# Performance work log

Hardware: AMD Instinct MI355X
Metric: run time of the kernel (lower is better)

The kernel has to match this reference:

```python
import jax, jax.numpy as jnp
import numpy as np
import math

B, T, C = 2, 1024, 1024
H = 16
HS = C // H          # head size 64
ROT = HS // 2        # rotary dims 32
TT = 1024            # ctx_len
FFN = 4 * C
EPS = 1e-6


def _layernorm(x, g, b):
    m = jnp.mean(x, -1, keepdims=True)
    v = jnp.mean((x - m) ** 2, -1, keepdims=True)
    return (x - m) * jax.lax.rsqrt(v + EPS) * g + b


def _time_shift_half(x):
    # ZeroPad2d((0,0,1,-1)) applied to first half of channels: shift by one step in time
    c = x.shape[-1]
    a = jnp.pad(x[:, :, : c // 2], ((0, 0), (1, 0), (0, 0)))[:, :-1, :]
    return jnp.concatenate([a, x[:, :, c // 2 :]], axis=-1)


def _rotate_half(x):
    x1, x2 = jnp.split(x, 2, axis=-1)
    return jnp.concatenate([-x2, x1], axis=-1)


def _rotary_cos_sin(t_len, rot, base):
    inv_freq = 1.0 / (base ** (jnp.arange(0, rot, 2, dtype=jnp.float32) / rot))
    freqs = jnp.arange(t_len, dtype=jnp.float32)[:, None] * inv_freq[None, :]
    emb = jnp.concatenate([freqs, freqs], axis=-1)  # (T, rot)
    return jnp.cos(emb), jnp.sin(emb)


def _build_w(time_w, time_alpha, time_beta, t_len):
    # faithful translation of the pad/tile/reshape circulant trick
    w = jnp.pad(time_w, ((0, 0), (0, TT)))            # (H, 2TT)
    w = jnp.tile(w, (1, TT))                          # (H, 2TT*TT)
    w = w[:, :-TT].reshape(-1, TT, 2 * TT - 1)        # (H, TT, 2TT-1)
    w = w[:, :, TT - 1 :]                             # (H, TT, TT)
    return w[:, :t_len, :t_len] * time_alpha[:, :, :t_len] * time_beta[:, :t_len, :]


def setup_inputs() -> dict:
    key = jax.random.key(0)
    ks = jax.random.split(key, 24)
    s = 0.02
    d = {
        "x": jax.random.normal(ks[0], (B, T, C), jnp.float32),
        "ln1_g": jnp.ones((C,), jnp.float32),
        "ln1_b": jnp.zeros((C,), jnp.float32),
        "Wq": jax.random.normal(ks[1], (C, C), jnp.float32) * s,
        "bq": jnp.zeros((C,), jnp.float32),
        "Wk": jax.random.normal(ks[2], (C, C), jnp.float32) * s,
        "bk": jnp.zeros((C,), jnp.float32),
        "Wv": jax.random.normal(ks[3], (C, C), jnp.float32) * s,
        "bv": jnp.zeros((C,), jnp.float32),
        "Wo": jax.random.normal(ks[4], (C, C), jnp.float32) * s,
        "bo": jnp.zeros((C,), jnp.float32),
        "time_w": 1.0 + 0.01 * jax.random.normal(ks[5], (H, TT), jnp.float32),
        "time_alpha": 1.0 + 0.01 * jax.random.normal(ks[6], (H, 1, TT), jnp.float32),
        "time_beta": 1.0 + 0.01 * jax.random.normal(ks[7], (H, TT, 1), jnp.float32),
        "time_gamma": 1.0 + 0.01 * jax.random.normal(ks[8], (TT, 1), jnp.float32),
        "Wmix": jnp.eye(H, dtype=jnp.float32) + 0.01 * jax.random.normal(ks[9], (H, H), jnp.float32),
        "ln2_g": jnp.ones((C,), jnp.float32),
        "ln2_b": jnp.zeros((C,), jnp.float32),
        "Wgk": jax.random.normal(ks[10], (C, FFN), jnp.float32) * s,
        "bgk": jnp.zeros((FFN,), jnp.float32),
        "Wgv": jax.random.normal(ks[11], (C, FFN), jnp.float32) * s,
        "bgv": jnp.zeros((FFN,), jnp.float32),
        "Wgw": jax.random.normal(ks[12], (FFN, C), jnp.float32) * s,
        "bgw": jnp.zeros((C,), jnp.float32),
    }
    return d


def _block(x, ln1_g, ln1_b, Wq, bq, Wk, bk, Wv, bv, Wo, bo,
           time_w, time_alpha, time_beta, time_gamma, Wmix,
           ln2_g, ln2_b, Wgk, bgk, Wgv, bgv, Wgw, bgw):
    b, t, c = x.shape
    # ---- MHA_pro attention sublayer (pre-LN residual) ----
    xs = _time_shift_half(_layernorm(x, ln1_g, ln1_b))
    q = (xs @ Wq + bq).reshape(b, t, H, HS).transpose(0, 2, 1, 3)  # bhtd
    k = (xs @ Wk + bk).reshape(b, t, H, HS).transpose(0, 2, 1, 3)
    v = (xs @ Wv + bv).reshape(b, t, H, HS).transpose(0, 2, 1, 3)
    qr, qp = q[..., :ROT], q[..., ROT:]
    kr, kp = k[..., :ROT], k[..., ROT:]
    cos, sin = _rotary_cos_sin(t, ROT, float(TT))  # base = ctx_len
    qr = qr * cos + _rotate_half(qr) * sin
    kr = kr * cos + _rotate_half(kr) * sin
    q = jnp.concatenate([qr, qp], axis=-1)
    k = jnp.concatenate([kr, kp], axis=-1)
    att = jnp.einsum("bhtd,bhud->bhtu", q, k) * (1.0 / math.sqrt(HS))
    causal = jnp.tril(jnp.ones((t, t), bool))
    att = jnp.where(causal, att, -jnp.inf)
    att = jax.nn.softmax(att, axis=-1)
    w = _build_w(time_w, time_alpha, time_beta, t)  # (H, T, T)
    att = att * w[None]
    att = jnp.einsum("ij,bjtu->bitu", Wmix, att)  # 1x1 conv head mix
    y = jnp.einsum("bhtu,bhud->bhtd", att, v)
    y = y.transpose(0, 2, 1, 3).reshape(b, t, c)
    y = (y @ Wo + bo) * time_gamma[:t, :]
    x = x + y
    # ---- GeGLU MLP sublayer (pre-LN residual) ----
    xm = _layernorm(x, ln2_g, ln2_b)
    kk = xm @ Wgk + bgk
    vv = xm @ Wgv + bgv
    y2 = (jax.nn.gelu(kk, approximate=False) * vv) @ Wgw + bgw
    return x + y2


def reference(x, ln1_g, ln1_b, Wq, bq, Wk, bk, Wv, bv, Wo, bo,
              time_w, time_alpha, time_beta, time_gamma, Wmix,
              ln2_g, ln2_b, Wgk, bgk, Wgv, bgv, Wgw, bgw):
    return _block(x, ln1_g, ln1_b, Wq, bq, Wk, bk, Wv, bv, Wo, bo,
                  time_w, time_alpha, time_beta, time_gamma, Wmix,
                  ln2_g, ln2_b, Wgk, bgk, Wgv, bgv, Wgw, bgw)
```

## Files before the change

kernel.cpp:

```cpp
#include <hip/hip_runtime.h>
#include <math.h>

typedef unsigned short u16;
typedef short s16x8 __attribute__((ext_vector_type(8)));
typedef float f32x4 __attribute__((ext_vector_type(4)));

#define TB 2
#define TSEQ 1024
#define CC 1024
#define NH 16
#define HSZ 64
#define FFN 4096
#define MROWS (TB*TSEQ)

#define GLOAD16(g, l) __builtin_amdgcn_global_load_lds( \
    (const __attribute__((address_space(1))) unsigned*)(g), \
    (__attribute__((address_space(3))) unsigned*)(l), 16, 0, 0)

#define SBAR()  __builtin_amdgcn_s_barrier()
#define SCHED0() __builtin_amdgcn_sched_barrier(0)
#define LGKM0() asm volatile("s_waitcnt lgkmcnt(0)" ::: "memory")
#define WAITV4() asm volatile("s_waitcnt vmcnt(4)" ::: "memory")
#define PRIO(n) __builtin_amdgcn_s_setprio(n)

__device__ __forceinline__ float bf2f(u16 u){
  union { unsigned u; float f; } c; c.u = ((unsigned)u) << 16; return c.f;
}
__device__ __forceinline__ u16 f2bf(float f){
  union { float f; unsigned u; } c; c.f = f;
  unsigned u = c.u;
  u += 0x7fffu + ((u >> 16) & 1);
  return (u16)(u >> 16);
}
__device__ __forceinline__ float ldin(const void* p, size_t i, int bf){
  return bf ? bf2f(((const u16*)p)[i]) : ((const float*)p)[i];
}

__global__ void k_flag(const unsigned* __restrict__ g, int* __restrict__ flag){
  if (threadIdx.x == 0) *flag = (g[0] == 0x3F800000u) ? 0 : 1;
}

struct Prep {
  const void* csrc[10]; u16* cdst[10]; int cp0[11];
  const void* tw; u16* tw8; float2* rt;
};
__global__ void k_prep(Prep P, const int* __restrict__ flagp){
  int bf = *flagp;
  int blk = blockIdx.x, tid = threadIdx.x;
  if (blk < 184){
    int idx = blk*256 + tid;
    int s = 0;
    #pragma unroll
    for (int i = 1; i < 10; i++) if (idx >= P.cp0[i]) s = i;
    int r = idx - P.cp0[s];
    P.cdst[s][r] = f2bf(ldin(P.csrc[s], r, bf));
  } else if (blk < 696){
    int idx = (blk-184)*256 + tid;
    int s = idx >> 14;
    int h = (idx >> 10) & 15;
    int k = idx & 1023;
    float v = (k + s < 1024) ? ldin(P.tw, h*1024 + k + s, bf) : 0.f;
    P.tw8[idx] = f2bf(v);
  } else {
    int idx = (blk-696)*256 + tid;
    int i = idx & 15, t = idx >> 4;
    float invf = exp2f(-0.625f * (float)i);
    float ang = (float)t * invf;
    P.rt[idx] = (float2){cosf(ang), sinf(ang)};
  }
}

struct TEnt { const void* src; u16* dst; int R, C, bxn, blk0; };
struct TPack { TEnt e[7]; };
__global__ void k_transpose_all(TPack p, const int* __restrict__ flagp){
  int bf = *flagp;
  __shared__ u16 tile[32][33];
  int blk = blockIdx.x;
  int ei = 0;
  #pragma unroll
  for (int i = 1; i < 7; i++) if (blk >= p.e[i].blk0) ei = i;
  const void* src = p.e[ei].src;
  u16* dst = p.e[ei].dst;
  int R = p.e[ei].R, C = p.e[ei].C;
  int rel = blk - p.e[ei].blk0;
  int bx = (rel % p.e[ei].bxn) * 32, by = (rel / p.e[ei].bxn) * 32;
  int tx = threadIdx.x & 31, ty = threadIdx.x >> 5;
  #pragma unroll
  for (int i = 0; i < 32; i += 8)
    tile[ty + i][tx] = f2bf(ldin(src, (size_t)(by + ty + i) * C + bx + tx, bf));
  __syncthreads();
  #pragma unroll
  for (int i = 0; i < 32; i += 8)
    dst[(size_t)(bx + ty + i) * R + by + tx] = tile[tx][ty + i];
}

__global__ void k_ln1_shift(const void* __restrict__ x, const void* __restrict__ g,
                            const void* __restrict__ bta, u16* __restrict__ xs,
                            const int* __restrict__ flagp){
  int bf = *flagp;
  int row = blockIdx.x;
  int t = row & (TSEQ - 1);
  int tid = threadIdx.x;
  int wv = tid >> 6, lane = tid & 63;
  float v[4]; float s = 0.f, ss = 0.f;
  #pragma unroll
  for (int i = 0; i < 4; i++){
    v[i] = ldin(x, (size_t)row * CC + tid*4 + i, bf);
    s += v[i]; ss += v[i]*v[i];
  }
  #pragma unroll
  for (int o = 32; o > 0; o >>= 1){ s += __shfl_xor(s, o); ss += __shfl_xor(ss, o); }
  __shared__ float rs[4], rss[4];
  if (lane == 0){ rs[wv] = s; rss[wv] = ss; }
  __syncthreads();
  float S = rs[0]+rs[1]+rs[2]+rs[3];
  float SS = rss[0]+rss[1]+rss[2]+rss[3];
  float mean = S * (1.0f/CC);
  float var  = SS * (1.0f/CC) - mean*mean;
  float inv  = rsqrtf(var + 1e-6f);
  #pragma unroll
  for (int i = 0; i < 4; i++){
    int c = tid*4 + i;
    float o = (v[i]-mean)*inv*ldin(g, c, bf) + ldin(bta, c, bf);
    u16 ob = f2bf(o);
    if (c >= CC/2)            xs[(size_t)row*CC + c] = ob;
    else if (t < TSEQ-1)      xs[(size_t)(row+1)*CC + c] = ob;
  }
  if (t == 0 && tid < 128){
    #pragma unroll
    for (int i = 0; i < 4; i++) xs[(size_t)row*CC + tid*4 + i] = 0;
  }
}

__global__ void k_ln2(const float* __restrict__ x1, const void* __restrict__ g,
                      const void* __restrict__ bta, u16* __restrict__ xm,
                      const int* __restrict__ flagp){
  int bf = *flagp;
  int row = blockIdx.x;
  int tid = threadIdx.x;
  int wv = tid >> 6, lane = tid & 63;
  const float* xr = x1 + (size_t)row * CC;
  float v[4]; float s = 0.f, ss = 0.f;
  #pragma unroll
  for (int i = 0; i < 4; i++){ v[i] = xr[tid*4 + i]; s += v[i]; ss += v[i]*v[i]; }
  #pragma unroll
  for (int o = 32; o > 0; o >>= 1){ s += __shfl_xor(s, o); ss += __shfl_xor(ss, o); }
  __shared__ float rs[4], rss[4];
  if (lane == 0){ rs[wv] = s; rss[wv] = ss; }
  __syncthreads();
  float S = rs[0]+rs[1]+rs[2]+rs[3];
  float SS = rss[0]+rss[1]+rss[2]+rss[3];
  float mean = S * (1.0f/CC);
  float var  = SS * (1.0f/CC) - mean*mean;
  float inv  = rsqrtf(var + 1e-6f);
  #pragma unroll
  for (int i = 0; i < 4; i++){
    int c = tid*4 + i;
    xm[(size_t)row*CC + c] = f2bf((v[i]-mean)*inv*ldin(g, c, bf) + ldin(bta, c, bf));
  }
}

__global__ void k_rotary(u16* __restrict__ qkv, const float2* __restrict__ rt){
  int idx = blockIdx.x*256 + threadIdx.x;
  int i = idx & 15;
  int h = (idx >> 4) & (NH-1);
  int row = idx >> 8;
  int t = row & (TSEQ-1);
  float2 cssn = rt[t*16 + i];
  float cs = cssn.x, sn = cssn.y;
  size_t base = (size_t)row * (3*CC);
  u16* qp = qkv + base + h*HSZ;
  float a = bf2f(qp[i]), b2 = bf2f(qp[i+16]);
  qp[i]    = f2bf(a*cs - b2*sn);
  qp[i+16] = f2bf(b2*cs + a*sn);
  u16* kp = qkv + base + CC + h*HSZ;
  a = bf2f(kp[i]); b2 = bf2f(kp[i+16]);
  kp[i]    = f2bf(a*cs - b2*sn);
  kp[i+16] = f2bf(b2*cs + a*sn);
}

__global__ __launch_bounds__(256) void k_qk(
    const u16* __restrict__ qkv, u16* __restrict__ att)
{
  int m0 = blockIdx.y * 128;
  int n0 = blockIdx.x * 128;
  if (n0 > m0) return;
  int bh = blockIdx.z; int b = bh >> 4, h = bh & 15;
  __shared__ u16 As[128*32];
  __shared__ u16 Bs[128*32];
  int tid = threadIdx.x;
  int w = tid >> 6;
  int lane = tid & 63;
  int wm = (w >> 1) * 64, wn = (w & 1) * 64;
  f32x4 acc[4][4];
  #pragma unroll
  for (int i = 0; i < 4; i++)
    #pragma unroll
    for (int j = 0; j < 4; j++) acc[i][j] = (f32x4){0.f,0.f,0.f,0.f};

  int rr = lane >> 2;
  int cc = lane & 3;
  const u16* gA0 = qkv + (size_t)(b*TSEQ + m0 + w*32 + rr)*(3*CC) + h*HSZ + cc*8;
  const u16* gA1 = gA0 + (size_t)16*(3*CC);
  const u16* gB0 = qkv + (size_t)(b*TSEQ + n0 + w*32 + rr)*(3*CC) + CC + h*HSZ + cc*8;
  const u16* gB1 = gB0 + (size_t)16*(3*CC);
  u16* lA0 = As + (w*32)*32;
  u16* lA1 = As + (w*32+16)*32;
  u16* lB0 = Bs + (w*32)*32;
  u16* lB1 = Bs + (w*32+16)*32;
  int quad = lane >> 4;
  int l15 = lane & 15;

  #pragma unroll
  for (int k0 = 0; k0 < HSZ; k0 += 32){
    __syncthreads();
    GLOAD16(gA0 + k0, lA0);
    GLOAD16(gA1 + k0, lA1);
    GLOAD16(gB0 + k0, lB0);
    GLOAD16(gB1 + k0, lB1);
    __syncthreads();
    s16x8 af[4], bfr[4];
    #pragma unroll
    for (int i = 0; i < 4; i++){
      af[i]  = *(s16x8*)&As[(wm + i*16 + l15)*32 + quad*8];
      bfr[i] = *(s16x8*)&Bs[(wn + i*16 + l15)*32 + quad*8];
    }
    #pragma unroll
    for (int mi = 0; mi < 4; mi++)
      #pragma unroll
      for (int ni = 0; ni < 4; ni++)
        acc[mi][ni] = __builtin_amdgcn_mfma_f32_16x16x32_bf16(af[mi], bfr[ni], acc[mi][ni], 0, 0, 0);
  }

  #pragma unroll
  for (int mi = 0; mi < 4; mi++){
    int rowb = m0 + wm + mi*16 + quad*4;
    #pragma unroll
    for (int ni = 0; ni < 4; ni++){
      int col = n0 + wn + ni*16 + l15;
      #pragma unroll
      for (int r = 0; r < 4; r++){
        int t = rowb + r;
        att[((size_t)bh*TSEQ + t)*TSEQ + col] = f2bf(acc[mi][ni][r] * 0.125f);
      }
    }
  }
}

__global__ __launch_bounds__(256) void k_softmix(
    u16* __restrict__ att, const u16* __restrict__ tw8, const u16* __restrict__ al16,
    const u16* __restrict__ be16, const void* __restrict__ wmix,
    const int* __restrict__ flagp)
{
  int bf = *flagp;
  int bt = blockIdx.x;
  int t = bt & (TSEQ-1);
  int b = bt >> 10;
  int tid = threadIdx.x;
  int wv = tid >> 6;
  int lane = tid & 63;
  int tile_end = ((t >> 7) + 1) << 7;
  int nchunk = (t >> 9) + 1;
  int sh = (TSEQ-1 - t) & 7;
  int base = (TSEQ-1 - t) - sh;
  __shared__ __align__(16) u16 P[NH][TSEQ];
  __shared__ float wm[NH*NH];
  if (tid < NH*NH) wm[tid] = ldin(wmix, tid, bf);

  #pragma unroll
  for (int hi = 0; hi < 4; hi++){
    int h = wv*4 + hi;
    const u16* srow = att + ((size_t)(b*NH + h)*TSEQ + t)*TSEQ;
    const u16* twp  = tw8 + ((size_t)sh*NH + h)*TSEQ + base;
    const u16* alp  = al16 + h*TSEQ;
    float v[16];
    float lmax = -1e30f;
    for (int r = 0; r < nchunk; r++){
      int ub = lane*8 + r*512;
      uint4 pk = *(const uint4*)(srow + ub);
      const u16* pe = (const u16*)&pk;
      #pragma unroll
      for (int e = 0; e < 8; e++){
        float s = bf2f(pe[e]);
        if (ub + e > t) s = -1e30f;
        v[r*8+e] = s;
        lmax = fmaxf(lmax, s);
      }
    }
    #pragma unroll
    for (int o = 32; o > 0; o >>= 1) lmax = fmaxf(lmax, __shfl_xor(lmax, o));
    float lsum = 0.f;
    for (int r = 0; r < nchunk; r++){
      #pragma unroll
      for (int e = 0; e < 8; e++){
        float p = __expf(v[r*8+e] - lmax);
        v[r*8+e] = p; lsum += p;
      }
    }
    #pragma unroll
    for (int o = 32; o > 0; o >>= 1) lsum += __shfl_xor(lsum, o);
    float btv = bf2f(be16[h*TSEQ + t]);
    float inv = btv / lsum;
    for (int r = 0; r < nchunk; r++){
      int ub = lane*8 + r*512;
      uint4 wk = *(const uint4*)(twp + ub);
      uint4 ak = *(const uint4*)(alp + ub);
      const u16* we = (const u16*)&wk;
      const u16* ae = (const u16*)&ak;
      u16 tmp[8];
      #pragma unroll
      for (int e = 0; e < 8; e++){
        float p = v[r*8+e] * inv * bf2f(we[e]) * bf2f(ae[e]);
        tmp[e] = f2bf(p);
      }
      *(uint4*)&P[h][ub] = *(uint4*)tmp;
    }
  }
  __syncthreads();

  int u0 = tid * 4;
  if (u0 < tile_end){
    #pragma unroll
    for (int half2 = 0; half2 < 2; half2++){
      float acc[8][4];
      #pragma unroll
      for (int i = 0; i < 8; i++)
        #pragma unroll
        for (int k = 0; k < 4; k++) acc[i][k] = 0.f;
      #pragma unroll
      for (int j = 0; j < 16; j++){
        uint2 pk = *(const uint2*)&P[j][u0];
        float p0 = bf2f((u16)(pk.x & 0xffff)), p1 = bf2f((u16)(pk.x >> 16));
        float p2 = bf2f((u16)(pk.y & 0xffff)), p3 = bf2f((u16)(pk.y >> 16));
        #pragma unroll
        for (int i2 = 0; i2 < 8; i2++){
          float w = wm[(half2*8 + i2)*NH + j];
          acc[i2][0] += w*p0; acc[i2][1] += w*p1; acc[i2][2] += w*p2; acc[i2][3] += w*p3;
        }
      }
      #pragma unroll
      for (int i2 = 0; i2 < 8; i2++){
        int i = half2*8 + i2;
        u16 tmp[4] = {f2bf(acc[i2][0]), f2bf(acc[i2][1]), f2bf(acc[i2][2]), f2bf(acc[i2][3])};
        *(uint2*)(att + ((size_t)(b*NH + i)*TSEQ + t)*TSEQ + u0) = *(uint2*)tmp;
      }
    }
  }
}

__global__ void k_vt(const u16* __restrict__ qkv, u16* __restrict__ vt){
  __shared__ u16 tile[32][33];
  int bh = blockIdx.z; int b = bh >> 4, h = bh & 15;
  int u0 = blockIdx.x * 32, d0 = blockIdx.y * 32;
  int tx = threadIdx.x & 31, ty = threadIdx.x >> 5;
  #pragma unroll
  for (int i = 0; i < 32; i += 8)
    tile[ty + i][tx] = qkv[(size_t)(b*TSEQ + u0 + ty + i)*(3*CC) + 2*CC + h*HSZ + d0 + tx];
  __syncthreads();
  #pragma unroll
  for (int i = 0; i < 32; i += 8)
    vt[((size_t)bh*HSZ + d0 + ty + i)*TSEQ + u0 + tx] = tile[tx][ty + i];
}

__global__ void k_gelumul(const u16* __restrict__ kkvv, u16* __restrict__ hh){
  int idx = blockIdx.x*256 + threadIdx.x;
  int m = idx >> 9;
  int j = (idx & 511) * 8;
  uint4 kk4 = *(const uint4*)(kkvv + (size_t)m*(2*FFN) + j);
  uint4 vv4 = *(const uint4*)(kkvv + (size_t)m*(2*FFN) + FFN + j);
  const u16* ks = (const u16*)&kk4;
  const u16* vs = (const u16*)&vv4;
  u16 out[8];
  #pragma unroll
  for (int e = 0; e < 8; e++){
    float kk = bf2f(ks[e]), vv = bf2f(vs[e]);
    float ge = 0.5f*kk*(1.0f + erff(kk*0.70710678f));
    out[e] = f2bf(ge*vv);
  }
  *(uint4*)(hh + (size_t)m*FFN + j) = *(uint4*)out;
}

__global__ __launch_bounds__(512, 2) void k_gemm256(
    const u16* __restrict__ A, const u16* __restrict__ Bt,
    const u16* __restrict__ bias, int M, int N, int K, int mode,
    u16* __restrict__ outp, float* __restrict__ partial)
{
  __shared__ u16 S[65536];
  u16* SA0 = S;
  u16* SB0 = S + 16384;
  u16* SA1 = S + 32768;
  u16* SB1 = S + 49152;

  int nwg = (int)(gridDim.x * gridDim.y * gridDim.z);
  int lin = (int)(blockIdx.x + gridDim.x * (blockIdx.y + gridDim.y * blockIdx.z));
  int nl  = (nwg & 7) ? lin : ((lin & 7) * (nwg >> 3) + (lin >> 3));
  int bx  = nl % (int)gridDim.x;
  int tq  = nl / (int)gridDim.x;
  int by  = tq % (int)gridDim.y;
  int bz  = tq / (int)gridDim.y;

  int m0 = by * 256, n0 = bx * 256;
  int kper = K / (int)gridDim.z;
  int kbeg = bz * kper;
  int nt = kper >> 6;
  int niter = nt >> 1;

  int tid = threadIdx.x;
  int w = tid >> 6, lane = tid & 63;
  int wm = w >> 2, wn = w & 3;
  int quad = lane >> 4, l15 = lane & 15;
  int l3 = lane >> 3, ch = (lane & 7) ^ l3;

  const u16* gA = A  + (size_t)(m0 + w*16 + l3) * K + ch*8 + kbeg;
  const u16* gB = Bt + (size_t)(n0 + w*16 + l3) * K + ch*8 + kbeg;
  const size_t hstep = (size_t)128 * K;
  const size_t rstep = (size_t)8 * K;

  int pc0 = quad ^ (l15 & 7);
  int pc1 = (4 + quad) ^ (l15 & 7);
  int aoff0 = (wm*128 + l15)*64 + pc0*8;
  int aoff1 = (wm*128 + l15)*64 + pc1*8;
  int boff0 = (wn*64 + l15)*64 + pc0*8;
  int boff1 = (wn*64 + l15)*64 + pc1*8;

  f32x4 acc[8][4];
  #pragma unroll
  for (int i = 0; i < 8; i++)
    #pragma unroll
    for (int j = 0; j < 4; j++) acc[i][j] = (f32x4){0.f,0.f,0.f,0.f};

  #define STG(gbase, sbase, h, ko) do{ \
      const u16* _g = (gbase) + (size_t)(h)*hstep + (ko); \
      u16* _l = (sbase) + ((h)*128 + w*16)*64; \
      GLOAD16(_g, _l); \
      GLOAD16(_g + rstep, _l + 512); \
    }while(0)

  #define LD_A(buf, MQ) do{ _Pragma("unroll") for (int _m = 0; _m < 4; _m++){ \
      a0[_m] = *(const s16x8*)((buf) + aoff0 + (MQ)*4096 + _m*1024); \
      a1[_m] = *(const s16x8*)((buf) + aoff1 + (MQ)*4096 + _m*1024); } }while(0)

  #define LD_B(buf, NQ, B0A, B1A) do{ _Pragma("unroll") for (int _n = 0; _n < 2; _n++){ \
      B0A[_n] = *(const s16x8*)((buf) + boff0 + (NQ)*2048 + _n*1024); \
      B1A[_n] = *(const s16x8*)((buf) + boff1 + (NQ)*2048 + _n*1024); } }while(0)

  #define MMQ(MQ, NQ, B0A, B1A) do{ _Pragma("unroll") for (int _m = 0; _m < 4; _m++){ \
      _Pragma("unroll") for (int _n = 0; _n < 2; _n++){ \
        acc[(MQ)*4+_m][(NQ)*2+_n] = __builtin_amdgcn_mfma_f32_16x16x32_bf16(a0[_m], B0A[_n], acc[(MQ)*4+_m][(NQ)*2+_n], 0, 0, 0); \
        acc[(MQ)*4+_m][(NQ)*2+_n] = __builtin_amdgcn_mfma_f32_16x16x32_bf16(a1[_m], B1A[_n], acc[(MQ)*4+_m][(NQ)*2+_n], 0, 0, 0); }} }while(0)

  STG(gB, SB0, 0, 0); STG(gB, SB0, 1, 0);
  STG(gA, SA0, 0, 0); STG(gA, SA0, 1, 0);
  STG(gB, SB1, 0, 64); STG(gB, SB1, 1, 64);
  WAITV4();
  SBAR();

  s16x8 a0[4], a1[4], bl0[2], bl1[2], bh0[2], bh1[2];

  for (int i = 0; i < niter; i++){
    int t1k = (2*i+1)*64;
    int t2k = (2*i+2 < nt) ? (2*i+2)*64 : 0;
    int t3k = (2*i+3 < nt) ? (2*i+3)*64 : 0;

    LD_A(SA0, 0); LD_B(SB0, 0, bl0, bl1);
    STG(gA, SA1, 0, t1k);
    SBAR(); LGKM0(); SCHED0(); PRIO(1); MMQ(0,0,bl0,bl1); PRIO(0); SBAR();
    LD_B(SB0, 1, bh0, bh1);
    STG(gA, SA1, 1, t1k);
    SBAR(); LGKM0(); SCHED0(); PRIO(1); MMQ(0,1,bh0,bh1); PRIO(0); SBAR();
    LD_A(SA0, 1);
    STG(gB, SB0, 0, t2k);
    SBAR(); LGKM0(); SCHED0(); PRIO(1); MMQ(1,0,bl0,bl1); PRIO(0); SBAR();
    STG(gB, SB0, 1, t2k);
    SBAR(); LGKM0(); SCHED0(); PRIO(1); MMQ(1,1,bh0,bh1); PRIO(0);
    WAITV4(); SBAR();
    LD_A(SA1, 0); LD_B(SB1, 0, bl0, bl1);
    STG(gA, SA0, 0, t2k);
    SBAR(); LGKM0(); SCHED0(); PRIO(1); MMQ(0,0,bl0,bl1); PRIO(0); SBAR();
    LD_B(SB1, 1, bh0, bh1);
    STG(gA, SA0, 1, t2k);
    SBAR(); LGKM0(); SCHED0(); PRIO(1); MMQ(0,1,bh0,bh1); PRIO(0); SBAR();
    LD_A(SA1, 1);
    STG(gB, SB1, 0, t3k);
    SBAR(); LGKM0(); SCHED0(); PRIO(1); MMQ(1,0,bl0,bl1); PRIO(0); SBAR();
    STG(gB, SB1, 1, t3k);
    SBAR(); LGKM0(); SCHED0(); PRIO(1); MMQ(1,1,bh0,bh1); PRIO(0);
    WAITV4(); SBAR();
  }

  if (mode == 3){
    float* pout = partial + (size_t)bz * M * N;
    #pragma unroll
    for (int mi = 0; mi < 8; mi++){
      int rowb = m0 + wm*128 + mi*16 + quad*4;
      #pragma unroll
      for (int ni = 0; ni < 4; ni++){
        int col = n0 + wn*64 + ni*16 + l15;
        #pragma unroll
        for (int r = 0; r < 4; r++)
          pout[(size_t)(rowb + r) * N + col] = acc[mi][ni][r];
      }
    }
  } else {
    #pragma unroll
    for (int mi = 0; mi < 8; mi++){
      int rowb = m0 + wm*128 + mi*16 + quad*4;
      #pragma unroll
      for (int ni = 0; ni < 4; ni++){
        int col = n0 + wn*64 + ni*16 + l15;
        float bv = bf2f(bias[col]);
        #pragma unroll
        for (int r = 0; r < 4; r++)
          outp[(size_t)(rowb + r) * N + col] = f2bf(acc[mi][ni][r] + bv);
      }
    }
  }
  #undef STG
  #undef LD_A
  #undef LD_B
  #undef MMQ
}

__global__ __launch_bounds__(256) void k_gemm(
    const u16* __restrict__ A, const u16* __restrict__ Bt,
    const u16* __restrict__ bias, int M, int N, int K, int mode,
    void* __restrict__ outp, const void* __restrict__ xres,
    const float* __restrict__ resf, const u16* __restrict__ gamma,
    float* __restrict__ partial, const int* __restrict__ flagp)
{
  int bf = *flagp;
  __shared__ u16 As[128*32];
  __shared__ u16 Bs[128*32];
  int tid = threadIdx.x;
  int m0 = blockIdx.y * 128;
  int n0 = blockIdx.x * 128;
  int nz = gridDim.z;
  int kper = K / nz;
  int kbeg = blockIdx.z * kper;
  int kend = kbeg + kper;
  int w = tid >> 6;
  int lane = tid & 63;
  int wm = (w >> 1) * 64, wn = (w & 1) * 64;
  f32x4 acc[4][4];
  #pragma unroll
  for (int i = 0; i < 4; i++)
    #pragma unroll
    for (int j = 0; j < 4; j++) acc[i][j] = (f32x4){0.f,0.f,0.f,0.f};

  int rr = lane >> 2;
  int cc = lane & 3;
  const u16* gA0 = A  + (size_t)(m0 + w*32 + rr)*K + cc*8;
  const u16* gA1 = gA0 + (size_t)16*K;
  const u16* gB0 = Bt + (size_t)(n0 + w*32 + rr)*K + cc*8;
  const u16* gB1 = gB0 + (size_t)16*K;
  u16* lA0 = As + (w*32)*32;
  u16* lA1 = As + (w*32+16)*32;
  u16* lB0 = Bs + (w*32)*32;
  u16* lB1 = Bs + (w*32+16)*32;
  int quad = lane >> 4;
  int l15 = lane & 15;

  for (int k0 = kbeg; k0 < kend; k0 += 32){
    __syncthreads();
    GLOAD16(gA0 + k0, lA0);
    GLOAD16(gA1 + k0, lA1);
    GLOAD16(gB0 + k0, lB0);
    GLOAD16(gB1 + k0, lB1);
    __syncthreads();
    s16x8 af[4], bfr[4];
    #pragma unroll
    for (int i = 0; i < 4; i++){
      af[i]  = *(s16x8*)&As[(wm + i*16 + l15)*32 + quad*8];
      bfr[i] = *(s16x8*)&Bs[(wn + i*16 + l15)*32 + quad*8];
    }
    #pragma unroll
    for (int mi = 0; mi < 4; mi++)
      #pragma unroll
      for (int ni = 0; ni < 4; ni++)
        acc[mi][ni] = __builtin_amdgcn_mfma_f32_16x16x32_bf16(af[mi], bfr[ni], acc[mi][ni], 0, 0, 0);
  }

  if (nz > 1){
    float* pout = partial + (size_t)blockIdx.z * M * N;
    #pragma unroll
    for (int mi = 0; mi < 4; mi++){
      int rowb = m0 + wm + mi*16 + quad*4;
      #pragma unroll
      for (int ni = 0; ni < 4; ni++){
        int col = n0 + wn + ni*16 + l15;
        #pragma unroll
        for (int r = 0; r < 4; r++)
          pout[(size_t)(rowb + r) * N + col] = acc[mi][ni][r];
      }
    }
    return;
  }

  #pragma unroll
  for (int mi = 0; mi < 4; mi++){
    int rowb = m0 + wm + mi*16 + quad*4;
    #pragma unroll
    for (int ni = 0; ni < 4; ni++){
      int col = n0 + wn + ni*16 + l15;
      float bv = bf2f(bias[col]);
      #pragma unroll
      for (int r = 0; r < 4; r++){
        int row = rowb + r;
        float val = acc[mi][ni][r] + bv;
        size_t idx = (size_t)row * N + col;
        if (mode == 0){
          ((u16*)outp)[idx] = f2bf(val);
        } else if (mode == 1){
          int t = row & (TSEQ-1);
          ((float*)outp)[idx] = ldin(xres, idx, bf) + val * bf2f(gamma[t]);
        } else {
          float o = resf[idx] + val;
          if (bf) ((u16*)outp)[idx] = f2bf(o);
          else    ((float*)outp)[idx] = o;
        }
      }
    }
  }
}

__global__ void k_reduceK(const float* __restrict__ partial, int nsplit,
                          int M, int N, const u16* __restrict__ bias, int mode,
                          void* __restrict__ outp, const void* __restrict__ xres,
                          const float* __restrict__ resf, const u16* __restrict__ gamma,
                          const int* __restrict__ flagp){
  int bf = *flagp;
  int idx = blockIdx.x*256 + threadIdx.x;
  int row = idx / (N/4);
  int c0  = (idx % (N/4)) * 4;
  size_t base = (size_t)row * N + c0;
  float v[4] = {0.f, 0.f, 0.f, 0.f};
  for (int s = 0; s < nsplit; s++){
    const float4 p = *(const float4*)(partial + (size_t)s * M * N + base);
    v[0] += p.x; v[1] += p.y; v[2] += p.z; v[3] += p.w;
  }
  #pragma unroll
  for (int e = 0; e < 4; e++) v[e] += bf2f(bias[c0 + e]);
  if (mode == 1){
    int t = row & (TSEQ-1);
    float gm = bf2f(gamma[t]);
    float o[4];
    #pragma unroll
    for (int e = 0; e < 4; e++) o[e] = ldin(xres, base + e, bf) + v[e] * gm;
    *(float4*)((float*)outp + base) = (float4){o[0], o[1], o[2], o[3]};
  } else {
    float o[4];
    #pragma unroll
    for (int e = 0; e < 4; e++) o[e] = resf[base + e] + v[e];
    if (bf){
      u16 tmp[4] = {f2bf(o[0]), f2bf(o[1]), f2bf(o[2]), f2bf(o[3])};
      *(uint2*)((u16*)outp + base) = *(uint2*)tmp;
    } else {
      *(float4*)((float*)outp + base) = (float4){o[0], o[1], o[2], o[3]};
    }
  }
}

__global__ __launch_bounds__(256) void k_pv(
    const u16* __restrict__ att, const u16* __restrict__ vt, u16* __restrict__ y)
{
  __shared__ u16 As[128*32];
  __shared__ u16 Bs[64*32];
  int tid = threadIdx.x;
  int bh = blockIdx.y; int b = bh >> 4, h = bh & 15;
  int m0 = blockIdx.x * 128;
  const u16* A  = att + (size_t)bh * TSEQ * TSEQ;
  const u16* Bt = vt  + (size_t)bh * HSZ * TSEQ;
  int w = tid >> 6;
  int lane = tid & 63;
  int wm = (w >> 1) * 64, wn = (w & 1) * 32;
  f32x4 acc[4][2];
  #pragma unroll
  for (int i = 0; i < 4; i++){ acc[i][0] = (f32x4){0,0,0,0}; acc[i][1] = (f32x4){0,0,0,0}; }

  int rr = lane >> 2;
  int cc = lane & 3;
  const u16* gA0 = A + (size_t)(m0 + w*32 + rr)*TSEQ + cc*8;
  const u16* gA1 = gA0 + (size_t)16*TSEQ;
  const u16* gB0 = Bt + (size_t)(w*16 + rr)*TSEQ + cc*8;
  u16* lA0 = As + (w*32)*32;
  u16* lA1 = As + (w*32+16)*32;
  u16* lB0 = Bs + (w*16)*32;
  int quad = lane >> 4;
  int l15 = lane & 15;
  int kend = m0 + 128;

  for (int k0 = 0; k0 < kend; k0 += 32){
    __syncthreads();
    GLOAD16(gA0 + k0, lA0);
    GLOAD16(gA1 + k0, lA1);
    GLOAD16(gB0 + k0, lB0);
    __syncthreads();
    s16x8 af[4], bfr[2];
    #pragma unroll
    for (int i = 0; i < 4; i++)
      af[i] = *(s16x8*)&As[(wm + i*16 + l15)*32 + quad*8];
    #pragma unroll
    for (int i = 0; i < 2; i++)
      bfr[i] = *(s16x8*)&Bs[(wn + i*16 + l15)*32 + quad*8];
    #pragma unroll
    for (int mi = 0; mi < 4; mi++)
      #pragma unroll
      for (int ni = 0; ni < 2; ni++)
        acc[mi][ni] = __builtin_amdgcn_mfma_f32_16x16x32_bf16(af[mi], bfr[ni], acc[mi][ni], 0, 0, 0);
  }

  #pragma unroll
  for (int mi = 0; mi < 4; mi++){
    int rowb = m0 + wm + mi*16 + quad*4;
    #pragma unroll
    for (int ni = 0; ni < 2; ni++){
      int col = wn + ni*16 + l15;
      #pragma unroll
      for (int r = 0; r < 4; r++){
        int t = rowb + r;
        y[(size_t)(b*TSEQ + t)*CC + h*HSZ + col] = f2bf(acc[mi][ni][r]);
      }
    }
  }
}

extern "C" void kernel_launch(void* const* d_in, const int* in_sizes, int n_in,
                              void* d_out, int out_size, void* d_ws, size_t ws_size,
                              hipStream_t stream){
  const void* x     = d_in[0];
  const void* ln1g  = d_in[1];
  const void* ln1b  = d_in[2];
  const void* Wq    = d_in[3];
  const void* bq    = d_in[4];
  const void* Wk    = d_in[5];
  const void* bk    = d_in[6];
  const void* Wv    = d_in[7];
  const void* bv    = d_in[8];
  const void* Wo    = d_in[9];
  const void* bo    = d_in[10];
  const void* timew = d_in[11];
  const void* alpha = d_in[12];
  const void* beta  = d_in[13];
  const void* gamma = d_in[14];
  const void* Wmix  = d_in[15];
  const void* ln2g  = d_in[16];
  const void* ln2b  = d_in[17];
  const void* Wgk   = d_in[18];
  const void* bgk   = d_in[19];
  const void* Wgv   = d_in[20];
  const void* bgv   = d_in[21];
  const void* Wgw   = d_in[22];
  const void* bgw   = d_in[23];

  char* ws = (char*)d_ws;
  size_t off = 0;
  auto carve = [&](size_t bytes)->char*{
    char* p = ws + off; off = (off + bytes + 255) & ~(size_t)255; return p;
  };
  int*  FLAG   = (int*)carve(256);
  u16*  WT_QKV = (u16*)carve(3072ull*1024*2);
  u16*  WT_O   = (u16*)carve(1024ull*1024*2);
  u16*  WT_G   = (u16*)carve(8192ull*1024*2);
  u16*  WT_W   = (u16*)carve(1024ull*4096*2);
  u16*  B_QKV  = (u16*)carve(3072*2);
  u16*  B_G    = (u16*)carve(8192*2);
  u16*  B_O    = (u16*)carve(1024*2);
  u16*  B_W    = (u16*)carve(1024*2);
  u16*  GMA    = (u16*)carve(1024*2);
  u16*  TW8    = (u16*)carve(8ull*16*1024*2 + 4096);
  u16*  AL16   = (u16*)carve(16*1024*2);
  u16*  BE16   = (u16*)carve(16*1024*2);
  u16*  XS     = (u16*)carve((size_t)MROWS*CC*2);
  u16*  QKV    = (u16*)carve((size_t)MROWS*3*CC*2);
  u16*  ATT    = (u16*)carve((size_t)TB*NH*TSEQ*TSEQ*2);
  u16*  VT     = (u16*)carve((size_t)TB*NH*HSZ*TSEQ*2);
  u16*  Y      = (u16*)carve((size_t)MROWS*CC*2);
  float* X1    = (float*)carve((size_t)MROWS*CC*4);
  u16*  XM     = (u16*)carve((size_t)MROWS*CC*2);
  u16*  KKVV   = (u16*)carve((size_t)MROWS*2*FFN*2);
  u16*  HH     = (u16*)carve((size_t)MROWS*FFN*2);
  float2* RT   = (float2*)carve((size_t)TSEQ*16*8);
  float* PART  = (float*)ATT;
  (void)ws_size; (void)in_sizes; (void)n_in; (void)out_size;

  k_flag<<<1,64,0,stream>>>((const unsigned*)ln1g, FLAG);

  Prep P;
  P.csrc[0]=bq;    P.cdst[0]=B_QKV;
  P.csrc[1]=bk;    P.cdst[1]=B_QKV+1024;
  P.csrc[2]=bv;    P.cdst[2]=B_QKV+2048;
  P.csrc[3]=bgk;   P.cdst[3]=B_G;
  P.csrc[4]=bgv;   P.cdst[4]=B_G+4096;
  P.csrc[5]=bo;    P.cdst[5]=B_O;
  P.csrc[6]=bgw;   P.cdst[6]=B_W;
  P.csrc[7]=gamma; P.cdst[7]=GMA;
  P.csrc[8]=alpha; P.cdst[8]=AL16;
  P.csrc[9]=beta;  P.cdst[9]=BE16;
  int sizes[10] = {1024,1024,1024,4096,4096,1024,1024,1024,16384,16384};
  int acc0 = 0;
  for (int i = 0; i < 10; i++){ P.cp0[i] = acc0; acc0 += sizes[i]; }
  P.cp0[10] = acc0;
  P.tw = timew; P.tw8 = TW8; P.rt = RT;
  k_prep<<<760,256,0,stream>>>(P, FLAG);

  TPack T;
  T.e[0] = {Wq,  WT_QKV,                1024, 1024,  32,     0};
  T.e[1] = {Wk,  WT_QKV + 1024*1024,    1024, 1024,  32,  1024};
  T.e[2] = {Wv,  WT_QKV + 2*1024*1024,  1024, 1024,  32,  2048};
  T.e[3] = {Wo,  WT_O,                  1024, 1024,  32,  3072};
  T.e[4] = {Wgk, WT_G,                  1024, 4096, 128,  4096};
  T.e[5] = {Wgv, WT_G + 4096ull*1024,   1024, 4096, 128,  8192};
  T.e[6] = {Wgw, WT_W,                  4096, 1024,  32, 12288};
  k_transpose_all<<<16384,256,0,stream>>>(T, FLAG);

  k_ln1_shift<<<MROWS,256,0,stream>>>(x, ln1g, ln1b, XS, FLAG);
  k_gemm256<<<dim3(12,8),512,0,stream>>>(XS, WT_QKV, B_QKV, MROWS, 3072, 1024, 0,
                                         QKV, nullptr);
  k_rotary<<<2048,256,0,stream>>>(QKV, RT);
  k_qk<<<dim3(8,8,TB*NH),256,0,stream>>>(QKV, ATT);
  k_softmix<<<TB*TSEQ,256,0,stream>>>(ATT, TW8, AL16, BE16, Wmix, FLAG);
  k_vt<<<dim3(32,2,32),256,0,stream>>>(QKV, VT);
  k_pv<<<dim3(8,32),256,0,stream>>>(ATT, VT, Y);

  k_gemm<<<dim3(8,16,2),256,0,stream>>>(Y, WT_O, B_O, MROWS, 1024, 1024, 1,
                                        nullptr, nullptr, nullptr, nullptr, PART, FLAG);
  k_reduceK<<<MROWS*1024/(4*256),256,0,stream>>>(PART, 2, MROWS, 1024, B_O, 1,
                                                 X1, x, nullptr, GMA, FLAG);

  k_ln2<<<MROWS,256,0,stream>>>(X1, ln2g, ln2b, XM, FLAG);
  k_gemm256<<<dim3(32,8),512,0,stream>>>(XM, WT_G, B_G, MROWS, 8192, 1024, 0,
                                         KKVV, nullptr);
  k_gelumul<<<(MROWS*FFN)/(256*8),256,0,stream>>>(KKVV, HH);

  k_gemm256<<<dim3(4,8,8),512,0,stream>>>(HH, WT_W, nullptr, MROWS, 1024, 4096, 3,
                                          nullptr, PART);
  k_reduceK<<<MROWS*1024/(4*256),256,0,stream>>>(PART, 8, MROWS, 1024, B_W, 2,
                                                 d_out, nullptr, X1, nullptr, FLAG);
}
```

Before: 406.8 us.

## Use one wavefront per head and one column per thread in softmix

Expands the softmix block to 1024 threads so each of the 16 heads gets its own wavefront for the softmax and weighting phase, instead of each wave looping over four heads. The head-mixing phase is remapped so each thread handles one column and produces all 16 mixed head outputs. This aims to raise parallelism and latency hiding per block. In exchange, per-thread stores shrink to 2-byte writes, and larger blocks may reduce scheduling flexibility and occupancy.

```diff
diff --git a/kernel.cpp b/kernel.cpp
--- a/kernel.cpp
+++ b/kernel.cpp
@@ -247,7 +247,7 @@
   }
 }
 
-__global__ __launch_bounds__(256) void k_softmix(
+__global__ __launch_bounds__(1024) void k_softmix(
     u16* __restrict__ att, const u16* __restrict__ tw8, const u16* __restrict__ al16,
     const u16* __restrict__ be16, const void* __restrict__ wmix,
     const int* __restrict__ flagp)
@@ -257,7 +257,7 @@
   int t = bt & (TSEQ-1);
   int b = bt >> 10;
   int tid = threadIdx.x;
-  int wv = tid >> 6;
+  int h = tid >> 6;
   int lane = tid & 63;
   int tile_end = ((t >> 7) + 1) << 7;
   int nchunk = (t >> 9) + 1;
@@ -267,9 +267,7 @@
   __shared__ float wm[NH*NH];
   if (tid < NH*NH) wm[tid] = ldin(wmix, tid, bf);
 
-  #pragma unroll
-  for (int hi = 0; hi < 4; hi++){
-    int h = wv*4 + hi;
+  {
     const u16* srow = att + ((size_t)(b*NH + h)*TSEQ + t)*TSEQ;
     const u16* twp  = tw8 + ((size_t)sh*NH + h)*TSEQ + base;
     const u16* alp  = al16 + h*TSEQ;
@@ -318,33 +316,20 @@
   }
   __syncthreads();
 
-  int u0 = tid * 4;
+  int u0 = tid;
   if (u0 < tile_end){
-    #pragma unroll
-    for (int half2 = 0; half2 < 2; half2++){
-      float acc[8][4];
-      #pragma unroll
-      for (int i = 0; i < 8; i++)
-        #pragma unroll
-        for (int k = 0; k < 4; k++) acc[i][k] = 0.f;
-      #pragma unroll
-      for (int j = 0; j < 16; j++){
-        uint2 pk = *(const uint2*)&P[j][u0];
-        float p0 = bf2f((u16)(pk.x & 0xffff)), p1 = bf2f((u16)(pk.x >> 16));
-        float p2 = bf2f((u16)(pk.y & 0xffff)), p3 = bf2f((u16)(pk.y >> 16));
-        #pragma unroll
-        for (int i2 = 0; i2 < 8; i2++){
-          float w = wm[(half2*8 + i2)*NH + j];
-          acc[i2][0] += w*p0; acc[i2][1] += w*p1; acc[i2][2] += w*p2; acc[i2][3] += w*p3;
-        }
-      }
-      #pragma unroll
-      for (int i2 = 0; i2 < 8; i2++){
-        int i = half2*8 + i2;
-        u16 tmp[4] = {f2bf(acc[i2][0]), f2bf(acc[i2][1]), f2bf(acc[i2][2]), f2bf(acc[i2][3])};
-        *(uint2*)(att + ((size_t)(b*NH + i)*TSEQ + t)*TSEQ + u0) = *(uint2*)tmp;
-      }
-    }
+    float acc[16];
+    #pragma unroll
+    for (int i = 0; i < 16; i++) acc[i] = 0.f;
+    #pragma unroll
+    for (int j = 0; j < 16; j++){
+      float p = bf2f(P[j][u0]);
+      #pragma unroll
+      for (int i = 0; i < 16; i++) acc[i] += wm[i*NH + j] * p;
+    }
+    #pragma unroll
+    for (int i = 0; i < 16; i++)
+      att[((size_t)(b*NH + i)*TSEQ + t)*TSEQ + u0] = f2bf(acc[i]);
   }
 }
 
@@ -818,7 +803,7 @@
                                          QKV, nullptr);
   k_rotary<<<2048,256,0,stream>>>(QKV, RT);
   k_qk<<<dim3(8,8,TB*NH),256,0,stream>>>(QKV, ATT);
-  k_softmix<<<TB*TSEQ,256,0,stream>>>(ATT, TW8, AL16, BE16, Wmix, FLAG);
+  k_softmix<<<TB*TSEQ,1024,0,stream>>>(ATT, TW8, AL16, BE16, Wmix, FLAG);
   k_vt<<<dim3(32,2,32),256,0,stream>>>(QKV, VT);
   k_pv<<<dim3(8,32),256,0,stream>>>(ATT, VT, Y);
 
```

Result: no change. 404.6 us (-0.5%).
